# Kernel optimization log

Measured on AMD Instinct MI355X. Metric: run time of the kernel, lower is better.

Reference implementation:

```python
import jax, jax.numpy as jnp
import numpy as np

D_IN = 2048
D_OUT = 2048
NUM_HEADS = 16
NUM_KV_GROUPS = 4
GROUP_SIZE = NUM_HEADS // NUM_KV_GROUPS  # 4
HEAD_DIM = D_OUT // NUM_HEADS            # 128


def setup_inputs() -> dict:
    key = jax.random.key(0)
    ks = jax.random.split(key, 6)
    b, n = 2, 2048
    x = jax.random.normal(ks[0], (b, n, D_IN), dtype=jnp.float32)
    # weights stored as [in, out] so that x @ W matches torch's x @ weight.T
    Wq = jax.random.normal(ks[1], (D_IN, D_OUT), dtype=jnp.float32) * (1.0 / np.sqrt(D_IN))
    Wk = jax.random.normal(ks[2], (D_IN, NUM_KV_GROUPS * HEAD_DIM), dtype=jnp.float32) * (1.0 / np.sqrt(D_IN))
    Wv = jax.random.normal(ks[3], (D_IN, NUM_KV_GROUPS * HEAD_DIM), dtype=jnp.float32) * (1.0 / np.sqrt(D_IN))
    Wo = jax.random.normal(ks[4], (D_OUT, D_OUT), dtype=jnp.float32) * (1.0 / np.sqrt(D_OUT))
    bo = jax.random.normal(ks[5], (D_OUT,), dtype=jnp.float32) * 0.01
    return {"x": x, "Wq": Wq, "Wk": Wk, "Wv": Wv, "Wo": Wo, "bo": bo}


def reference(x, Wq, Wk, Wv, Wo, bo):
    b, n, _ = x.shape
    # projections
    q = (x @ Wq).reshape(b, n, NUM_KV_GROUPS, GROUP_SIZE, HEAD_DIM)  # [b,n,g,s,d]
    k = (x @ Wk).reshape(b, n, NUM_KV_GROUPS, HEAD_DIM)              # [b,n,g,d]
    v = (x @ Wv).reshape(b, n, NUM_KV_GROUPS, HEAD_DIM)
    scale = 1.0 / np.sqrt(HEAD_DIM).astype(np.float32)
    # scores: each group of GROUP_SIZE query heads shares one K/V head
    scores = jnp.einsum('bqgsd,bkgd->bgsqk', q, k) * scale  # [b,g,s,n,n]
    causal = jnp.arange(n)[:, None] < jnp.arange(n)[None, :]  # True above diagonal
    scores = jnp.where(causal, -jnp.inf, scores)
    attn = jax.nn.softmax(scores, axis=-1)
    # dropout omitted for determinism (eval-mode equivalent)
    ctx = jnp.einsum('bgsqk,bkgd->bqgsd', attn, v)  # [b,n,g,s,d]
    ctx = ctx.reshape(b, n, D_OUT)
    return ctx @ Wo + bo
```

## Files before the change

### kernel.cpp

```cpp
#include <hip/hip_runtime.h>
#include <hip/hip_bf16.h>

typedef short bf16x8 __attribute__((ext_vector_type(8)));
typedef float f32x4 __attribute__((ext_vector_type(4)));
typedef float f32x16 __attribute__((ext_vector_type(16)));
typedef unsigned int u32x4 __attribute__((ext_vector_type(4)));

#define MFMA16(a, b, c) __builtin_amdgcn_mfma_f32_16x16x32_bf16((a), (b), (c), 0, 0, 0)
#define MFMA32(a, b, c) __builtin_amdgcn_mfma_f32_32x32x16_bf16((a), (b), (c), 0, 0, 0)

static __device__ __forceinline__ unsigned short f2bf(float f) {
  union { float f; unsigned u; } v;
  v.f = f;
  unsigned r = (v.u + 0x7FFFu + ((v.u >> 16) & 1u)) >> 16;
  return (unsigned short)r;
}

static __device__ __forceinline__ void gload16(const void* g, void* l) {
  __builtin_amdgcn_global_load_lds(
      (const __attribute__((address_space(1))) unsigned int*)g,
      (__attribute__((address_space(3))) unsigned int*)l, 16, 0, 0);
}

__global__ __launch_bounds__(256) void cast_f32_bf16(
    const float* __restrict__ src, unsigned short* __restrict__ dst, int n4) {
  int stride = gridDim.x * blockDim.x;
  for (int i = blockIdx.x * blockDim.x + threadIdx.x; i < n4; i += stride) {
    float4 v = reinterpret_cast<const float4*>(src)[i];
    ushort4 o;
    o.x = f2bf(v.x); o.y = f2bf(v.y); o.z = f2bf(v.z); o.w = f2bf(v.w);
    reinterpret_cast<ushort4*>(dst)[i] = o;
  }
}

__global__ __launch_bounds__(256) void transpose_cast(
    const float* __restrict__ src, unsigned short* __restrict__ dst, int R, int C) {
  __shared__ float tile[32][33];
  int tx = threadIdx.x & 31;
  int ty = threadIdx.x >> 5;
  int r0 = blockIdx.y * 32, c0 = blockIdx.x * 32;
#pragma unroll
  for (int i = 0; i < 32; i += 8)
    tile[ty + i][tx] = src[(size_t)(r0 + ty + i) * C + (c0 + tx)];
  __syncthreads();
#pragma unroll
  for (int i = 0; i < 32; i += 8)
    dst[(size_t)(c0 + ty + i) * R + (r0 + tx)] = f2bf(tile[tx][ty + i]);
}

template <int EPI>
static __device__ __forceinline__ void gemm_core(
    unsigned short* Asm, unsigned short* Bsm,
    const unsigned short* __restrict__ A, const unsigned short* __restrict__ B,
    unsigned short* __restrict__ Cb, float* __restrict__ Cf,
    const float* __restrict__ bias, int N, int K, int bid) {
  const int tid = threadIdx.x;
  const int wave = tid >> 6;
  const int lane = tid & 63;
  const int l15 = lane & 15, l4 = lane >> 4;
  const int tilesN = N >> 7;
  const int bm = bid / tilesN, bn = bid % tilesN;
  const int row0 = bm << 7, col0 = bn << 7;
  const int wr = (wave >> 1) << 6, wc = (wave & 1) << 6;

  const int ch0 = wave * 128 + lane;
  const int ch1 = ch0 + 64;
  const int r_a0 = ch0 >> 2, k_a0 = (ch0 & 3) * 8;
  const int r_a1 = ch1 >> 2, k_a1 = (ch1 & 3) * 8;

  f32x4 acc[4][4] = {};

  for (int kt = 0; kt < K; kt += 32) {
    if (kt) __syncthreads();
    gload16(A + (size_t)(row0 + r_a0) * K + kt + k_a0, &Asm[(wave * 2 + 0) * 512]);
    gload16(A + (size_t)(row0 + r_a1) * K + kt + k_a1, &Asm[(wave * 2 + 1) * 512]);
    gload16(B + (size_t)(col0 + r_a0) * K + kt + k_a0, &Bsm[(wave * 2 + 0) * 512]);
    gload16(B + (size_t)(col0 + r_a1) * K + kt + k_a1, &Bsm[(wave * 2 + 1) * 512]);
    __syncthreads();

    bf16x8 af[4], bvf[4];
#pragma unroll
    for (int m = 0; m < 4; ++m)
      af[m] = *(const bf16x8*)&Asm[(wr + m * 16 + l15) * 32 + l4 * 8];
#pragma unroll
    for (int n = 0; n < 4; ++n)
      bvf[n] = *(const bf16x8*)&Bsm[(wc + n * 16 + l15) * 32 + l4 * 8];
#pragma unroll
    for (int m = 0; m < 4; ++m)
#pragma unroll
      for (int n = 0; n < 4; ++n)
        acc[m][n] = MFMA16(af[m], bvf[n], acc[m][n]);
  }

#pragma unroll
  for (int m = 0; m < 4; ++m) {
#pragma unroll
    for (int n = 0; n < 4; ++n) {
      int row = row0 + wr + m * 16 + l4 * 4;
      int col = col0 + wc + n * 16 + l15;
#pragma unroll
      for (int r = 0; r < 4; ++r) {
        if (EPI == 0) {
          Cb[(size_t)(row + r) * N + col] = f2bf(acc[m][n][r]);
        } else {
          Cf[(size_t)(row + r) * N + col] = acc[m][n][r] + bias[col];
        }
      }
    }
  }
}

template <int EPI>
__global__ __launch_bounds__(256) void gemm_bt(
    const unsigned short* __restrict__ A, const unsigned short* __restrict__ B,
    unsigned short* __restrict__ Cb, float* __restrict__ Cf,
    const float* __restrict__ bias, int N, int K) {
  __shared__ unsigned short Asm[128 * 32];
  __shared__ unsigned short Bsm[128 * 32];
  gemm_core<EPI>(Asm, Bsm, A, B, Cb, Cf, bias, N, K, blockIdx.x);
}

__global__ __launch_bounds__(256) void gemm_dual(
    const unsigned short* __restrict__ A1, const unsigned short* __restrict__ B1,
    unsigned short* __restrict__ C1,
    const unsigned short* __restrict__ A2, const unsigned short* __restrict__ B2,
    unsigned short* __restrict__ C2, int K) {
  __shared__ unsigned short Asm[128 * 32];
  __shared__ unsigned short Bsm[128 * 32];
  if (blockIdx.x < 128)
    gemm_core<0>(Asm, Bsm, A1, B1, C1, nullptr, nullptr, 512, K, blockIdx.x);
  else
    gemm_core<0>(Asm, Bsm, A2, B2, C2, nullptr, nullptr, 4096, K, blockIdx.x - 128);
}

__global__ __launch_bounds__(512, 2) void flash_gqa3(
    const unsigned short* __restrict__ Qb, const unsigned short* __restrict__ Kb,
    const unsigned short* __restrict__ VT, unsigned short* __restrict__ Ctx) {
  __shared__ unsigned short Ksm[2][64 * 128];
  __shared__ unsigned short Vsm[2][128 * 64];

  const int tid = threadIdx.x;
  const int wave = tid >> 6, lane = tid & 63;
  const int l31 = lane & 31, hi = lane >> 5;
  const int j = blockIdx.x;
  const int bg = blockIdx.y;
  const int b = bg >> 2, g = bg & 3;
  const int h = (g << 2) | (wave & 3);
  const int qt = (wave < 4) ? j : (63 - j);
  const int q0 = qt << 5;
  const int n_my = ((qt * 32 + 31) >> 6) + 1;
  const int n_tot = (((63 - j) * 32 + 31) >> 6) + 1;

  bf16x8 qf[8];
  {
    const unsigned short* qp =
        Qb + (size_t)(b * 2048 + q0 + l31) * 2048 + h * 128 + hi * 8;
#pragma unroll
    for (int ds = 0; ds < 8; ++ds) qf[ds] = *(const bf16x8*)(qp + ds * 16);
  }

  const int rK0 = tid >> 4, cK = tid & 15, rK1 = rK0 + 32;
  const unsigned short* kS0 =
      Kb + (size_t)(b * 2048 + rK0) * 512 + g * 128 + (cK ^ (rK0 & 7)) * 8;
  const unsigned short* kS1 =
      Kb + (size_t)(b * 2048 + rK1) * 512 + g * 128 + (cK ^ (rK1 & 7)) * 8;
  const int rV0 = tid >> 3, cV = tid & 7, rV1 = rV0 + 64;
  const unsigned short* vS0 =
      VT + (size_t)(g * 128 + rV0) * 4096 + b * 2048 + (cV ^ (rV0 & 7)) * 8;
  const unsigned short* vS1 =
      VT + (size_t)(g * 128 + rV1) * 4096 + b * 2048 + (cV ^ (rV1 & 7)) * 8;

  float m_r = -1e30f, l_r = 0.f;
  f32x16 o0 = {}, o1 = {}, o2 = {}, o3 = {};
  const float scale = 0.08838834764831845f;

#define STAGE(kvn, bufi)                                            \
  {                                                                 \
    unsigned short* kb_ = &Ksm[bufi][0];                            \
    unsigned short* vb_ = &Vsm[bufi][0];                            \
    gload16(kS0 + (size_t)(kvn)*512, kb_ + wave * 512);             \
    gload16(kS1 + (size_t)(kvn)*512, kb_ + 4096 + wave * 512);      \
    gload16(vS0 + (kvn), vb_ + wave * 512);                         \
    gload16(vS1 + (kvn), vb_ + 4096 + wave * 512);                  \
  }

  STAGE(0, 0);
  __syncthreads();

  for (int it = 0; it < n_tot; ++it) {
    const int kv = it << 6;
    if (it + 1 < n_tot) STAGE(kv + 64, (it + 1) & 1);
    if (it < n_my) {
      const char* Kl = (const char*)&Ksm[it & 1][0];
      const char* Vl = (const char*)&Vsm[it & 1][0];
      f32x16 st0 = {}, st1 = {};
#pragma unroll
      for (int ds = 0; ds < 8; ++ds) {
        const int c = ds * 32 + hi * 16;
        const int by0 = (l31 * 256 + c) ^ ((l31 & 7) << 4);
        const int by1 = ((32 + l31) * 256 + c) ^ ((l31 & 7) << 4);
        bf16x8 kf0 = *(const bf16x8*)(Kl + by0);
        bf16x8 kf1 = *(const bf16x8*)(Kl + by1);
        st0 = MFMA32(kf0, qf[ds], st0);
        st1 = MFMA32(kf1, qf[ds], st1);
      }
      const int q_abs = q0 + l31;
      if (kv + 64 > q0) {
#pragma unroll
        for (int r = 0; r < 16; ++r) {
          const int koff = (r & 3) + 8 * (r >> 2) + 4 * hi;
          st0[r] = (kv + koff <= q_abs) ? st0[r] * scale : -1e30f;
          st1[r] = (kv + 32 + koff <= q_abs) ? st1[r] * scale : -1e30f;
        }
      } else {
#pragma unroll
        for (int r = 0; r < 16; ++r) { st0[r] *= scale; st1[r] *= scale; }
      }
      float pm = st0[0];
#pragma unroll
      for (int r = 1; r < 16; ++r) pm = fmaxf(pm, st0[r]);
#pragma unroll
      for (int r = 0; r < 16; ++r) pm = fmaxf(pm, st1[r]);
      pm = fmaxf(pm, __shfl_xor(pm, 32));
      const float mn = fmaxf(m_r, pm);
      const float osc = __expf(m_r - mn);
      m_r = mn;
      l_r *= osc;
#pragma unroll
      for (int r = 0; r < 16; ++r) {
        o0[r] *= osc; o1[r] *= osc; o2[r] *= osc; o3[r] *= osc;
      }
      float ps = 0.f;
#pragma unroll
      for (int r = 0; r < 16; ++r) { st0[r] = __expf(st0[r] - mn); ps += st0[r]; }
#pragma unroll
      for (int r = 0; r < 16; ++r) { st1[r] = __expf(st1[r] - mn); ps += st1[r]; }
      ps += __shfl_xor(ps, 32);
      l_r += ps;
      unsigned w0[8], w1[8];
#pragma unroll
      for (int rp = 0; rp < 8; ++rp) {
        w0[rp] = (unsigned)f2bf(st0[2 * rp]) | ((unsigned)f2bf(st0[2 * rp + 1]) << 16);
        w1[rp] = (unsigned)f2bf(st1[2 * rp]) | ((unsigned)f2bf(st1[2 * rp + 1]) << 16);
      }
#define PV_KS(ks, W)                                                          \
      {                                                                       \
        const int k4 = ((ks) & 1) * 4;                                        \
        unsigned a0 = W[k4], a1 = W[k4 + 1], b0 = W[k4 + 2], b1 = W[k4 + 3];  \
        unsigned q0_ = hi ? a0 : b0, q1_ = hi ? a1 : b1;                      \
        unsigned e0 = (unsigned)__shfl_xor((int)q0_, 32);                     \
        unsigned e1 = (unsigned)__shfl_xor((int)q1_, 32);                     \
        union { u32x4 u; bf16x8 v; } pk;                                      \
        pk.u[0] = hi ? e0 : a0; pk.u[1] = hi ? e1 : a1;                       \
        pk.u[2] = hi ? b0 : e0; pk.u[3] = hi ? b1 : e1;                       \
        const int cb = (ks)*32 + hi * 16;                                     \
        { const int row = l31;      const int by = (row * 128 + cb) ^ ((row & 7) << 4); \
          bf16x8 vf = *(const bf16x8*)(Vl + by); o0 = MFMA32(vf, pk.v, o0); } \
        { const int row = 32 + l31; const int by = (row * 128 + cb) ^ ((row & 7) << 4); \
          bf16x8 vf = *(const bf16x8*)(Vl + by); o1 = MFMA32(vf, pk.v, o1); } \
        { const int row = 64 + l31; const int by = (row * 128 + cb) ^ ((row & 7) << 4); \
          bf16x8 vf = *(const bf16x8*)(Vl + by); o2 = MFMA32(vf, pk.v, o2); } \
        { const int row = 96 + l31; const int by = (row * 128 + cb) ^ ((row & 7) << 4); \
          bf16x8 vf = *(const bf16x8*)(Vl + by); o3 = MFMA32(vf, pk.v, o3); } \
      }
      PV_KS(0, w0) PV_KS(1, w0) PV_KS(2, w1) PV_KS(3, w1)
#undef PV_KS
    }
    __syncthreads();
  }
#undef STAGE

  const float inv = 1.f / l_r;
  unsigned short* cp = Ctx + (size_t)(b * 2048 + q0 + l31) * 2048 + h * 128;
#pragma unroll
  for (int a = 0; a < 4; ++a) {
    ushort4 p0, p1, p2, p3;
    p0.x = f2bf(o0[4 * a + 0] * inv); p0.y = f2bf(o0[4 * a + 1] * inv);
    p0.z = f2bf(o0[4 * a + 2] * inv); p0.w = f2bf(o0[4 * a + 3] * inv);
    p1.x = f2bf(o1[4 * a + 0] * inv); p1.y = f2bf(o1[4 * a + 1] * inv);
    p1.z = f2bf(o1[4 * a + 2] * inv); p1.w = f2bf(o1[4 * a + 3] * inv);
    p2.x = f2bf(o2[4 * a + 0] * inv); p2.y = f2bf(o2[4 * a + 1] * inv);
    p2.z = f2bf(o2[4 * a + 2] * inv); p2.w = f2bf(o2[4 * a + 3] * inv);
    p3.x = f2bf(o3[4 * a + 0] * inv); p3.y = f2bf(o3[4 * a + 1] * inv);
    p3.z = f2bf(o3[4 * a + 2] * inv); p3.w = f2bf(o3[4 * a + 3] * inv);
    const int cc = 8 * a + 4 * hi;
    *(ushort4*)(cp + 0 * 32 + cc) = p0;
    *(ushort4*)(cp + 1 * 32 + cc) = p1;
    *(ushort4*)(cp + 2 * 32 + cc) = p2;
    *(ushort4*)(cp + 3 * 32 + cc) = p3;
  }
}

extern "C" void kernel_launch(void* const* d_in, const int* in_sizes, int n_in,
                              void* d_out, int out_size, void* d_ws, size_t ws_size,
                              hipStream_t stream) {
  (void)in_sizes; (void)n_in; (void)out_size; (void)ws_size;
  const float* x  = (const float*)d_in[0];
  const float* Wq = (const float*)d_in[1];
  const float* Wk = (const float*)d_in[2];
  const float* Wv = (const float*)d_in[3];
  const float* Wo = (const float*)d_in[4];
  const float* bo = (const float*)d_in[5];
  float* out = (float*)d_out;

  unsigned short* Xb  = (unsigned short*)d_ws;
  unsigned short* WqT = Xb  + (size_t)4096 * 2048;
  unsigned short* WkT = WqT + (size_t)2048 * 2048;
  unsigned short* WvT = WkT + (size_t)512 * 2048;
  unsigned short* WoT = WvT + (size_t)512 * 2048;
  unsigned short* Qb  = WoT + (size_t)2048 * 2048;
  unsigned short* Kb  = Qb  + (size_t)4096 * 2048;
  unsigned short* VTb = Kb  + (size_t)4096 * 512;
  unsigned short* Ctx = VTb + (size_t)512 * 4096;

  cast_f32_bf16<<<2048, 256, 0, stream>>>(x, Xb, (4096 * 2048) / 4);
  transpose_cast<<<dim3(64, 64), 256, 0, stream>>>(Wq, WqT, 2048, 2048);
  transpose_cast<<<dim3(16, 64), 256, 0, stream>>>(Wk, WkT, 2048, 512);
  transpose_cast<<<dim3(16, 64), 256, 0, stream>>>(Wv, WvT, 2048, 512);
  transpose_cast<<<dim3(64, 64), 256, 0, stream>>>(Wo, WoT, 2048, 2048);

  gemm_bt<0><<<dim3(512), 256, 0, stream>>>(Xb, WqT, Qb, nullptr, nullptr, 2048, 2048);
  gemm_dual<<<dim3(256), 256, 0, stream>>>(Xb, WkT, Kb, WvT, Xb, VTb, 2048);

  flash_gqa3<<<dim3(32, 8), 512, 0, stream>>>(Qb, Kb, VTb, Ctx);

  gemm_bt<1><<<dim3(512), 256, 0, stream>>>(Ctx, WoT, nullptr, out, bo, 2048, 2048);
}
```

Baseline: 233.0 us.

## Add 8-wave triple-buffered GEMM and lazy softmax rescaling with MFMA priority

Replaces the 128x128 4-wave GEMM used for the Q and output projections with a 256x128 tile, 8-wave kernel. It uses BK=64, three LDS buffers, split half-stage prefetches, explicit vmcnt waits and s_setprio around the MFMA blocks, so that global loads overlap compute. In the flash attention kernel it raises wave priority around the MFMA sections. It also skips the online-softmax rescale of the O accumulator unless the running max grows by more than 8, accepting exp values up to e^8 before normalization. The larger tiles yield only 256 blocks, and the deferred rescale relies on fp32 headroom.

```diff
diff --git a/kernel.cpp b/kernel.cpp
--- a/kernel.cpp
+++ b/kernel.cpp
@@ -110,16 +110,6 @@
   }
 }
 
-template <int EPI>
-__global__ __launch_bounds__(256) void gemm_bt(
-    const unsigned short* __restrict__ A, const unsigned short* __restrict__ B,
-    unsigned short* __restrict__ Cb, float* __restrict__ Cf,
-    const float* __restrict__ bias, int N, int K) {
-  __shared__ unsigned short Asm[128 * 32];
-  __shared__ unsigned short Bsm[128 * 32];
-  gemm_core<EPI>(Asm, Bsm, A, B, Cb, Cf, bias, N, K, blockIdx.x);
-}
-
 __global__ __launch_bounds__(256) void gemm_dual(
     const unsigned short* __restrict__ A1, const unsigned short* __restrict__ B1,
     unsigned short* __restrict__ C1,
@@ -133,6 +123,134 @@
     gemm_core<0>(Asm, Bsm, A2, B2, C2, nullptr, nullptr, 4096, K, blockIdx.x - 128);
 }
 
+template <int EPI>
+__global__ __launch_bounds__(512, 2) void gemm8p(
+    const unsigned short* __restrict__ A, const unsigned short* __restrict__ B,
+    unsigned short* __restrict__ Cb, float* __restrict__ Cf,
+    const float* __restrict__ bias, int N, int K) {
+  __shared__ unsigned short Al[3][256 * 64];
+  __shared__ unsigned short Bl[3][128 * 64];
+  const int tid = threadIdx.x;
+  const int wave = tid >> 6, lane = tid & 63;
+  const int l15 = lane & 15, l4 = lane >> 4;
+  const int tilesN = N >> 7;
+  const int bm = blockIdx.x / tilesN, bn = blockIdx.x % tilesN;
+  const int row0 = bm << 8, col0 = bn << 7;
+  const int wr = (wave >> 1) << 6;
+  const int wc = (wave & 1) << 6;
+
+  const unsigned short* sA[4];
+  const unsigned short* sB[2];
+#pragma unroll
+  for (int i = 0; i < 4; ++i) {
+    int q = i * 512 + wave * 64 + lane;
+    int r = q >> 3, c = (q & 7) ^ (r & 7);
+    sA[i] = A + (size_t)(row0 + r) * K + c * 8;
+  }
+#pragma unroll
+  for (int i = 0; i < 2; ++i) {
+    int q = i * 512 + wave * 64 + lane;
+    int r = q >> 3, c = (q & 7) ^ (r & 7);
+    sB[i] = B + (size_t)(col0 + r) * K + c * 8;
+  }
+
+#define STG_H1(t_, bi)                                             \
+  { const size_t ko = (size_t)(t_) * 64;                           \
+    gload16(sA[0] + ko, &Al[bi][(0 * 512 + wave * 64) * 8]);       \
+    gload16(sA[1] + ko, &Al[bi][(1 * 512 + wave * 64) * 8]);       \
+    gload16(sB[0] + ko, &Bl[bi][(0 * 512 + wave * 64) * 8]); }
+#define STG_H2(t_, bi)                                             \
+  { const size_t ko = (size_t)(t_) * 64;                           \
+    gload16(sA[2] + ko, &Al[bi][(2 * 512 + wave * 64) * 8]);       \
+    gload16(sA[3] + ko, &Al[bi][(3 * 512 + wave * 64) * 8]);       \
+    gload16(sB[1] + ko, &Bl[bi][(1 * 512 + wave * 64) * 8]); }
+
+  const int sw = l15 & 7;
+  const int c0 = (l4 ^ sw) << 4;
+  const int c1 = ((4 + l4) ^ sw) << 4;
+  const int rbA = (wr + l15) << 7;
+  const int rbB = (wc + l15) << 7;
+
+  f32x4 acc[4][4] = {};
+  const int NT = K >> 6;
+
+  STG_H1(0, 0); STG_H2(0, 0);
+  STG_H1(1, 1); STG_H2(1, 1);
+
+  int cur = 0;
+  for (int t = 0; t < NT; ++t) {
+    int sb = cur + 2; if (sb >= 3) sb -= 3;
+    if (t + 1 < NT) { asm volatile("s_waitcnt vmcnt(6)" ::: "memory"); }
+    else            { asm volatile("s_waitcnt vmcnt(0)" ::: "memory"); }
+    __builtin_amdgcn_s_barrier();
+    asm volatile("" ::: "memory");
+    const char* Ab = (const char*)&Al[cur][0];
+    const char* Bb = (const char*)&Bl[cur][0];
+    bf16x8 b0[4], b1[4], aA[2][2], aB[2][2];
+#pragma unroll
+    for (int n = 0; n < 4; ++n) {
+      b0[n] = *(const bf16x8*)(Bb + rbB + n * 2048 + c0);
+      b1[n] = *(const bf16x8*)(Bb + rbB + n * 2048 + c1);
+    }
+#pragma unroll
+    for (int m = 0; m < 2; ++m) {
+      aA[m][0] = *(const bf16x8*)(Ab + rbA + m * 2048 + c0);
+      aA[m][1] = *(const bf16x8*)(Ab + rbA + m * 2048 + c1);
+    }
+    if (t + 2 < NT) STG_H1(t + 2, sb);
+    asm volatile("" ::: "memory");
+    __builtin_amdgcn_s_barrier();
+    asm volatile("" ::: "memory");
+    __builtin_amdgcn_s_setprio(1);
+#pragma unroll
+    for (int m = 0; m < 2; ++m)
+#pragma unroll
+      for (int n = 0; n < 4; ++n) {
+        acc[m][n] = MFMA16(aA[m][0], b0[n], acc[m][n]);
+        acc[m][n] = MFMA16(aA[m][1], b1[n], acc[m][n]);
+      }
+    __builtin_amdgcn_s_setprio(0);
+#pragma unroll
+    for (int m = 0; m < 2; ++m) {
+      aB[m][0] = *(const bf16x8*)(Ab + rbA + (m + 2) * 2048 + c0);
+      aB[m][1] = *(const bf16x8*)(Ab + rbA + (m + 2) * 2048 + c1);
+    }
+    if (t + 2 < NT) STG_H2(t + 2, sb);
+    asm volatile("" ::: "memory");
+    __builtin_amdgcn_s_barrier();
+    asm volatile("" ::: "memory");
+    __builtin_amdgcn_s_setprio(1);
+#pragma unroll
+    for (int m = 0; m < 2; ++m)
+#pragma unroll
+      for (int n = 0; n < 4; ++n) {
+        acc[m + 2][n] = MFMA16(aB[m][0], b0[n], acc[m + 2][n]);
+        acc[m + 2][n] = MFMA16(aB[m][1], b1[n], acc[m + 2][n]);
+      }
+    __builtin_amdgcn_s_setprio(0);
+    cur += 1; if (cur >= 3) cur = 0;
+  }
+#undef STG_H1
+#undef STG_H2
+
+#pragma unroll
+  for (int m = 0; m < 4; ++m) {
+#pragma unroll
+    for (int n = 0; n < 4; ++n) {
+      int row = row0 + wr + m * 16 + l4 * 4;
+      int col = col0 + wc + n * 16 + l15;
+#pragma unroll
+      for (int r = 0; r < 4; ++r) {
+        if (EPI == 0) {
+          Cb[(size_t)(row + r) * N + col] = f2bf(acc[m][n][r]);
+        } else {
+          Cf[(size_t)(row + r) * N + col] = acc[m][n][r] + bias[col];
+        }
+      }
+    }
+  }
+}
+
 __global__ __launch_bounds__(512, 2) void flash_gqa3(
     const unsigned short* __restrict__ Qb, const unsigned short* __restrict__ Kb,
     const unsigned short* __restrict__ VT, unsigned short* __restrict__ Ctx) {
@@ -194,6 +312,7 @@
       const char* Kl = (const char*)&Ksm[it & 1][0];
       const char* Vl = (const char*)&Vsm[it & 1][0];
       f32x16 st0 = {}, st1 = {};
+      __builtin_amdgcn_s_setprio(1);
 #pragma unroll
       for (int ds = 0; ds < 8; ++ds) {
         const int c = ds * 32 + hi * 16;
@@ -204,6 +323,7 @@
         st0 = MFMA32(kf0, qf[ds], st0);
         st1 = MFMA32(kf1, qf[ds], st1);
       }
+      __builtin_amdgcn_s_setprio(0);
       const int q_abs = q0 + l31;
       if (kv + 64 > q0) {
 #pragma unroll
@@ -222,19 +342,21 @@
 #pragma unroll
       for (int r = 0; r < 16; ++r) pm = fmaxf(pm, st1[r]);
       pm = fmaxf(pm, __shfl_xor(pm, 32));
-      const float mn = fmaxf(m_r, pm);
-      const float osc = __expf(m_r - mn);
-      m_r = mn;
-      l_r *= osc;
-#pragma unroll
-      for (int r = 0; r < 16; ++r) {
-        o0[r] *= osc; o1[r] *= osc; o2[r] *= osc; o3[r] *= osc;
+      if (!__all(pm - m_r <= 8.0f)) {
+        const float mn = fmaxf(m_r, pm);
+        const float osc = __expf(m_r - mn);
+        m_r = mn;
+        l_r *= osc;
+#pragma unroll
+        for (int r = 0; r < 16; ++r) {
+          o0[r] *= osc; o1[r] *= osc; o2[r] *= osc; o3[r] *= osc;
+        }
       }
       float ps = 0.f;
 #pragma unroll
-      for (int r = 0; r < 16; ++r) { st0[r] = __expf(st0[r] - mn); ps += st0[r]; }
-#pragma unroll
-      for (int r = 0; r < 16; ++r) { st1[r] = __expf(st1[r] - mn); ps += st1[r]; }
+      for (int r = 0; r < 16; ++r) { st0[r] = __expf(st0[r] - m_r); ps += st0[r]; }
+#pragma unroll
+      for (int r = 0; r < 16; ++r) { st1[r] = __expf(st1[r] - m_r); ps += st1[r]; }
       ps += __shfl_xor(ps, 32);
       l_r += ps;
       unsigned w0[8], w1[8];
@@ -243,6 +365,7 @@
         w0[rp] = (unsigned)f2bf(st0[2 * rp]) | ((unsigned)f2bf(st0[2 * rp + 1]) << 16);
         w1[rp] = (unsigned)f2bf(st1[2 * rp]) | ((unsigned)f2bf(st1[2 * rp + 1]) << 16);
       }
+      __builtin_amdgcn_s_setprio(1);
 #define PV_KS(ks, W)                                                          \
       {                                                                       \
         const int k4 = ((ks) & 1) * 4;                                        \
@@ -265,6 +388,7 @@
       }
       PV_KS(0, w0) PV_KS(1, w0) PV_KS(2, w1) PV_KS(3, w1)
 #undef PV_KS
+      __builtin_amdgcn_s_setprio(0);
     }
     __syncthreads();
   }
@@ -319,10 +443,10 @@
   transpose_cast<<<dim3(16, 64), 256, 0, stream>>>(Wv, WvT, 2048, 512);
   transpose_cast<<<dim3(64, 64), 256, 0, stream>>>(Wo, WoT, 2048, 2048);
 
-  gemm_bt<0><<<dim3(512), 256, 0, stream>>>(Xb, WqT, Qb, nullptr, nullptr, 2048, 2048);
+  gemm8p<0><<<dim3(256), 512, 0, stream>>>(Xb, WqT, Qb, nullptr, nullptr, 2048, 2048);
   gemm_dual<<<dim3(256), 256, 0, stream>>>(Xb, WkT, Kb, WvT, Xb, VTb, 2048);
 
   flash_gqa3<<<dim3(32, 8), 512, 0, stream>>>(Qb, Kb, VTb, Ctx);
 
-  gemm_bt<1><<<dim3(512), 256, 0, stream>>>(Ctx, WoT, nullptr, out, bo, 2048, 2048);
-}
+  gemm8p<1><<<dim3(256), 512, 0, stream>>>(Ctx, WoT, nullptr, out, bo, 2048, 2048);
+}
```

New measurement: 217.2 us. 1.07x faster.
